# Kernel optimization log

Measured on AMD Instinct MI355X. Metric: run time of the kernel, lower is better.

## Reference

```python
import jax, jax.numpy as jnp
import numpy as np

B, T, H, L, V = 256, 201, 512, 3, 100
SOS_IDX = 1


def setup_inputs() -> dict:
    key = jax.random.key(0)
    ks = jax.random.split(key, 9)
    s = 1.0 / np.sqrt(H)  # torch LSTM init scale
    return {
        "feat": jax.random.normal(ks[0], (B, H), jnp.float32),
        "target_seq": jax.random.randint(ks[1], (B, T), 0, V, jnp.int64),
        "embed": jax.random.normal(ks[2], (V, H), jnp.float32) * 0.02,
        "W_ih": jax.random.uniform(ks[3], (L, 4 * H, H), jnp.float32, -s, s),
        "W_hh": jax.random.uniform(ks[4], (L, 4 * H, H), jnp.float32, -s, s),
        "b_ih": jax.random.uniform(ks[5], (L, 4 * H), jnp.float32, -s, s),
        "b_hh": jax.random.uniform(ks[6], (L, 4 * H), jnp.float32, -s, s),
        "proj_W": jax.random.normal(ks[7], (V, H), jnp.float32) * 0.02,
        "proj_b": jnp.zeros((V,), jnp.float32),
    }


def reference(feat, target_seq, embed, W_ih, W_hh, b_ih, b_hh, proj_W, proj_b):
    n_layers = W_ih.shape[0]
    bsz = feat.shape[0]
    hid = feat.shape[1]

    # hidden init = resnet feature repeated across layers; cell = zeros
    h0 = jnp.broadcast_to(feat[None], (n_layers, bsz, hid))
    c0 = jnp.zeros_like(h0)

    # teacher forcing: embed target tokens for t = 1..T-1 -> [T-1, B, H]
    x_seq = embed[target_seq[:, 1:].T]

    def step(carry, x_t):
        h, c = carry  # [L, B, H] each
        inp = x_t
        h_new, c_new = [], []
        for l in range(n_layers):  # static small loop over layers
            gates = inp @ W_ih[l].T + b_ih[l] + h[l] @ W_hh[l].T + b_hh[l]
            i, f, g, o = jnp.split(gates, 4, axis=-1)  # torch gate order ifgo
            cl = jax.nn.sigmoid(f) * c[l] + jax.nn.sigmoid(i) * jnp.tanh(g)
            hl = jax.nn.sigmoid(o) * jnp.tanh(cl)
            h_new.append(hl)
            c_new.append(cl)
            inp = hl
        return (jnp.stack(h_new), jnp.stack(c_new)), inp

    _, outs = jax.lax.scan(step, (h0, c0), x_seq)  # outs: [T-1, B, H]

    # first output slot is the raw SOS embedding (as in the torch code)
    start = jnp.broadcast_to(embed[SOS_IDX][None, None, :], (1, bsz, hid))
    res = jnp.concatenate([start, outs], axis=0)  # [T, B, H]
    res = jnp.transpose(res, (1, 0, 2))           # [B, T, H]
    logits = res @ proj_W.T + proj_b              # [B, T, V]
    return jnp.transpose(logits, (0, 2, 1))       # [B, V, T]
```

## Files before the change

kernel.cpp:

```cpp
#include <hip/hip_runtime.h>
#include <hip/hip_bf16.h>
#include <stdint.h>

typedef __attribute__((ext_vector_type(8))) __bf16 bf16x8;
typedef __attribute__((ext_vector_type(8))) short short8;
typedef __attribute__((ext_vector_type(4))) float f32x4;
typedef __attribute__((ext_vector_type(16))) float f32x16;

#define NB 256
#define NT 201
#define NTS 200
#define NH 512
#define NV 100
#define NG 2048
#define NK2 1024

static __device__ __forceinline__ unsigned short f2bf(float f) {
  union { float f; uint32_t u; } v; v.f = f;
  uint32_t u = v.u;
  return (unsigned short)((u + 0x7fffu + ((u >> 16) & 1u)) >> 16);
}

__global__ void prep_kernel(const float* __restrict__ Wih, const float* __restrict__ Whh,
                            const float* __restrict__ bih, const float* __restrict__ bhh,
                            const float* __restrict__ projW, const float* __restrict__ embed,
                            const float* __restrict__ feat,
                            unsigned short* __restrict__ Wr, float* __restrict__ br,
                            unsigned short* __restrict__ WpB, unsigned short* __restrict__ sos,
                            unsigned short* __restrict__ hfeat)
{
  int idx = blockIdx.x * 256 + threadIdx.x;
  if (idx < 786432) {
    int l = idx >> 18;
    int rem = idx & 262143;
    int col = rem >> 7;
    int ch = rem & 127;
    int g = col & 3, j = col >> 2;
    int srow = g * 512 + j;
    int k0 = ch * 8;
    const float* src = (k0 < 512) ? (Wih + ((size_t)l * NG + srow) * NH + k0)
                                  : (Whh + ((size_t)l * NG + srow) * NH + (k0 - 512));
    union { short8 v; unsigned short u[8]; } o;
#pragma unroll
    for (int q = 0; q < 8; ++q) o.u[q] = f2bf(src[q]);
    *reinterpret_cast<short8*>(Wr + ((size_t)l * NG + col) * NK2 + k0) = o.v;
  } else if (idx < 792576) {
    int e = idx - 786432;
    int l = e >> 11;
    int col = e & 2047;
    int srow = (col & 3) * 512 + (col >> 2);
    br[e] = bih[l * NG + srow] + bhh[l * NG + srow];
  } else if (idx < 799744) {
    int e = idx - 792576;
    int row = e >> 6, sl = e & 63;
    int k0 = sl * 8;
    union { short8 v; unsigned short u[8]; } o;
    if (row < NV) {
      const float* src = projW + (size_t)row * NH + k0;
#pragma unroll
      for (int q = 0; q < 8; ++q) o.u[q] = f2bf(src[q]);
    } else {
#pragma unroll
      for (int q = 0; q < 8; ++q) o.u[q] = 0;
    }
    *reinterpret_cast<short8*>(WpB + (size_t)row * NH + k0) = o.v;
  } else if (idx < 799808) {
    int e = idx - 799744;
    int k0 = e * 8;
    union { short8 v; unsigned short u[8]; } o;
#pragma unroll
    for (int q = 0; q < 8; ++q) o.u[q] = f2bf(embed[NH + k0 + q]);
    *reinterpret_cast<short8*>(sos + k0) = o.v;
  } else if (idx < 816192) {
    int e = idx - 799808;
    int k0 = e * 8;
    union { short8 v; unsigned short u[8]; } o;
#pragma unroll
    for (int q = 0; q < 8; ++q) o.u[q] = f2bf(feat[k0 + q]);
    *reinterpret_cast<short8*>(hfeat + k0) = o.v;
  }
}

__global__ void embed_kernel(const int* __restrict__ tgt, const float* __restrict__ embed,
                             unsigned short* __restrict__ xemb)
{
  int idx = blockIdx.x * 256 + threadIdx.x;
  int r = idx >> 6, ch = idx & 63;
  int t = r >> 8, b = r & 255;
  int tok = tgt[b * NT + t + 1];
  const float* src = embed + (size_t)tok * NH + ch * 8;
  union { short8 v; unsigned short u[8]; } o;
#pragma unroll
  for (int q = 0; q < 8; ++q) o.u[q] = f2bf(src[q]);
  *reinterpret_cast<short8*>(xemb + (size_t)r * NH + ch * 8) = o.v;
}

template<int I, bool DEV>
struct Iss {
  static __device__ __forceinline__ void go(bf16x8* f, const unsigned short* p) {
    if constexpr (DEV)
      asm volatile("global_load_dwordx4 %0, %1, off offset:%c2 sc1"
                   : "=v"(f[I]) : "v"(p), "i"(I * 32));
    else
      asm volatile("global_load_dwordx4 %0, %1, off offset:%c2"
                   : "=v"(f[I]) : "v"(p), "i"(I * 32));
    Iss<I + 1, DEV>::go(f, p);
  }
};
template<bool DEV>
struct Iss<32, DEV> { static __device__ __forceinline__ void go(bf16x8*, const unsigned short*) {} };

static __device__ __forceinline__ unsigned ld_poll(const unsigned* p) {
  unsigned r;
  asm volatile("global_load_dword %0, %1, off sc1\n\ts_waitcnt vmcnt(0)"
               : "=v"(r) : "v"(p) : "memory");
  return r;
}

static __device__ __forceinline__ void sig_add(unsigned* p) {
  unsigned one = 1u;
  asm volatile("global_atomic_add %0, %1, off sc1" :: "v"(p), "v"(one) : "memory");
}

static __device__ __forceinline__ void stsc1(unsigned short* p, unsigned short v) {
  asm volatile("global_store_short %0, %1, off sc1" :: "v"(p), "v"(v) : "memory");
}

#define MFMA __builtin_amdgcn_mfma_f32_32x32x16_bf16
#define GW(N) do { asm volatile("s_waitcnt vmcnt(" #N ")"); \
                   __builtin_amdgcn_sched_barrier(0); } while (0)
#define VMCNT0 asm volatile("s_waitcnt vmcnt(0)" ::: "memory")

__global__ __launch_bounds__(128, 1)
void lstm_scan(const unsigned short* __restrict__ Wr, const float* __restrict__ br,
               const unsigned short* __restrict__ xemb, unsigned short* __restrict__ out0,
               unsigned short* __restrict__ out1, const unsigned short* __restrict__ hfeat,
               unsigned* __restrict__ bar)
{
  extern __shared__ char lds[];
  const int bid = blockIdx.x;
  const int c = bid & 7, wgi = bid >> 3;
  const int tid = threadIdx.x;
  const int wv = tid >> 6, l = tid & 63;
  const int lm = l & 31, lh = l >> 5;
  const int lh16 = lh * 16, lh8 = lh * 8;
  const int sampG = c * 32 + lm;
  const int colL = wv * 32 + lm;
  const int colG = wgi * 64 + colL;
  const bool isg = ((colG & 3) == 2);
  const int j = colG >> 2;
  const int xorr = (colL & 7) << 4;
  const char* wbase = lds + colL * 2048;
  unsigned* barc = bar + c * 64;

  const unsigned short* xs_[3] = { xemb, out0, out1 };
  unsigned short* os_[3] = { out0, out1, out0 };

  bf16x8 f[32];
  f32x16 a0a, a0b, a1a, a1b;

#define XM(ks) \
  a0a = MFMA(f[ks],     *(const bf16x8*)(wbase + (((ks)*32 + lh16) ^ xorr)),     a0a, 0,0,0); \
  a0b = MFMA(f[(ks)+1], *(const bf16x8*)(wbase + ((((ks)+1)*32 + lh16) ^ xorr)), a0b, 0,0,0);
#define HM(ks) \
  a1a = MFMA(f[ks],     *(const bf16x8*)(wbase + ((1024 + (ks)*32 + lh16) ^ xorr)),     a1a, 0,0,0); \
  a1b = MFMA(f[(ks)+1], *(const bf16x8*)(wbase + ((1024 + ((ks)+1)*32 + lh16) ^ xorr)), a1b, 0,0,0);

  for (int layer = 0; layer < 3; ++layer) {
    __syncthreads();
    if (layer == 2) __threadfence();
    const unsigned short* wsrc = Wr + ((size_t)layer * NG + (size_t)wgi * 64) * NK2;
    for (int e = tid; e < 8192; e += 128) {
      int row = e >> 7, sl = e & 127;
      int byte = row * 2048 + ((sl * 16) ^ ((row & 7) << 4));
      *reinterpret_cast<short8*>(lds + byte) =
          *reinterpret_cast<const short8*>(wsrc + (size_t)row * NK2 + sl * 8);
    }
    __syncthreads();

    const float bias = br[layer * NG + colG];
    float cst[16];
#pragma unroll
    for (int r = 0; r < 16; ++r) cst[r] = 0.f;

    const unsigned short* xsrc = xs_[layer];
    unsigned short* osrc = os_[layer];

    Iss<0, false>::go(f, xsrc + (size_t)sampG * NH + lh8);
#pragma unroll
    for (int i = 0; i < 16; ++i) { a0a[i] = 0.f; a0b[i] = 0.f; }
    GW(24); XM(0) XM(2) XM(4) XM(6)
    GW(16); XM(8) XM(10) XM(12) XM(14)
    GW(8);  XM(16) XM(18) XM(20) XM(22)
    GW(0);  XM(24) XM(26) XM(28) XM(30)

    for (int t = 0; t < NTS; ++t) {
      if (t) {
        unsigned tgt = 32u * (unsigned)(layer * NTS + t);
        while (ld_poll(barc) < tgt) {}
      }
      const unsigned short* hr = (t == 0)
          ? (hfeat + (size_t)sampG * NH + lh8)
          : (osrc + ((size_t)(t - 1) * NB + sampG) * NH + lh8);
      Iss<0, true>::go(f, hr);
#pragma unroll
      for (int i = 0; i < 16; ++i) { a1a[i] = 0.f; a1b[i] = 0.f; }
      GW(24); HM(0) HM(2) HM(4) HM(6)
      GW(16); HM(8) HM(10) HM(12) HM(14)
      GW(8);  HM(16) HM(18) HM(20) HM(22)
      GW(0);  HM(24) HM(26) HM(28) HM(30)

      unsigned short* orow = osrc + (size_t)t * NB * NH;
#pragma unroll
      for (int r = 0; r < 16; ++r) {
        float x = a0a[r] + a0b[r] + a1a[r] + a1b[r] + bias;
        float xx = isg ? (x + x) : x;
        float sgm = 1.f / (1.f + __expf(-xx));
        float a = isg ? (sgm + sgm - 1.f) : sgm;
        float f1 = __shfl_xor(a, 1);
        float u2 = __shfl_xor(a, 2);
        float o3 = __shfl_xor(a, 3);
        float cn = __builtin_fmaf(f1, cst[r], a * u2);
        cst[r] = cn;
        float e2 = __expf(-2.f * cn);
        float th = 2.f / (1.f + e2) - 1.f;
        float hv = o3 * th;
        if ((l & 3) == 0) {
          int m = (r & 3) + 8 * (r >> 2) + 4 * lh;
          stsc1(orow + (size_t)(c * 32 + m) * NH + j, f2bf(hv));
        }
      }

      VMCNT0;
      __syncthreads();
      if (tid == 0) sig_add(barc);

      if (t < NTS - 1) {
        Iss<0, false>::go(f, xsrc + ((size_t)(t + 1) * NB + sampG) * NH + lh8);
#pragma unroll
        for (int i = 0; i < 16; ++i) { a0a[i] = 0.f; a0b[i] = 0.f; }
        GW(24); XM(0) XM(2) XM(4) XM(6)
        GW(16); XM(8) XM(10) XM(12) XM(14)
        GW(8);  XM(16) XM(18) XM(20) XM(22)
        GW(0);  XM(24) XM(26) XM(28) XM(30)
      }
    }
  }
}

__global__ __launch_bounds__(256)
void proj_kernel(const unsigned short* __restrict__ WpB, const unsigned short* __restrict__ outL,
                 const unsigned short* __restrict__ sos, const float* __restrict__ pb,
                 float* __restrict__ dout)
{
  extern __shared__ char plds[];
  const int b = blockIdx.x, tid = threadIdx.x;
  const int wv = tid >> 6, l = tid & 63;
  const int ln = l & 15, lk = l >> 4;
  for (int e = tid; e < 7168; e += 256) {
    int row = e >> 6, sl = e & 63;
    int byte = row * 1024 + ((sl * 16) ^ ((row & 7) << 4));
    *reinterpret_cast<short8*>(plds + byte) =
        *reinterpret_cast<const short8*>(WpB + (size_t)row * NH + sl * 8);
  }
  __syncthreads();
  for (int nt = wv; nt < 13; nt += 4) {
    int tt = nt * 16 + ln;
    const unsigned short* rowp = (tt == 0 || tt > 200) ? sos
        : outL + ((size_t)(tt - 1) * NB + b) * NH;
    bf16x8 Bfr[16];
#pragma unroll
    for (int ks = 0; ks < 16; ++ks)
      Bfr[ks] = *reinterpret_cast<const bf16x8*>(rowp + ks * 32 + lk * 8);
    for (int mt = 0; mt < 7; ++mt) {
      f32x4 acc;
#pragma unroll
      for (int i = 0; i < 4; ++i) acc[i] = 0.f;
#pragma unroll
      for (int ks = 0; ks < 16; ++ks) {
        int row = mt * 16 + ln;
        int byte = row * 1024 + (((ks * 64) + lk * 16) ^ ((row & 7) << 4));
        bf16x8 a = *reinterpret_cast<const bf16x8*>(plds + byte);
        acc = __builtin_amdgcn_mfma_f32_16x16x32_bf16(a, Bfr[ks], acc, 0, 0, 0);
      }
#pragma unroll
      for (int r = 0; r < 4; ++r) {
        int v = mt * 16 + lk * 4 + r;
        if (v < NV && tt < NT)
          dout[((size_t)b * NV + v) * NT + tt] = acc[r] + pb[v];
      }
    }
  }
}

extern "C" void kernel_launch(void* const* d_in, const int* in_sizes, int n_in,
                              void* d_out, int out_size, void* d_ws, size_t ws_size,
                              hipStream_t stream)
{
  const float* feat  = (const float*)d_in[0];
  const int*   tgt   = (const int*)  d_in[1];
  const float* embed = (const float*)d_in[2];
  const float* Wih   = (const float*)d_in[3];
  const float* Whh   = (const float*)d_in[4];
  const float* bih   = (const float*)d_in[5];
  const float* bhh   = (const float*)d_in[6];
  const float* projW = (const float*)d_in[7];
  const float* pb    = (const float*)d_in[8];
  float* out = (float*)d_out;

  char* ws = (char*)d_ws;
  size_t off = 0;
  auto alloc = [&](size_t bytes) {
    char* p = ws + off;
    off = (off + bytes + 255) & ~(size_t)255;
    return p;
  };
  unsigned short* Wr    = (unsigned short*)alloc((size_t)3 * NG * NK2 * 2);
  float*          br    = (float*)         alloc((size_t)3 * NG * 4);
  unsigned short* WpB   = (unsigned short*)alloc((size_t)112 * NH * 2);
  unsigned short* sos   = (unsigned short*)alloc((size_t)NH * 2);
  unsigned short* hfeat = (unsigned short*)alloc((size_t)NB * NH * 2);
  unsigned short* xemb  = (unsigned short*)alloc((size_t)NTS * NB * NH * 2);
  unsigned short* out0  = (unsigned short*)alloc((size_t)NTS * NB * NH * 2);
  unsigned*       bar   = (unsigned*)      alloc(2048);
  unsigned short* out1 = xemb;

  hipMemsetAsync(bar, 0, 2048, stream);

  hipFuncSetAttribute((const void*)lstm_scan, hipFuncAttributeMaxDynamicSharedMemorySize, 131072);
  hipFuncSetAttribute((const void*)proj_kernel, hipFuncAttributeMaxDynamicSharedMemorySize, 114688);

  prep_kernel<<<3189, 256, 0, stream>>>(Wih, Whh, bih, bhh, projW, embed, feat,
                                        Wr, br, WpB, sos, hfeat);
  embed_kernel<<<12800, 256, 0, stream>>>(tgt, embed, xemb);
  lstm_scan<<<256, 128, 131072, stream>>>(Wr, br, xemb, out0, out1, hfeat, bar);
  proj_kernel<<<256, 256, 114688, stream>>>(WpB, out0, sos, pb, out);
}
```

Baseline: 4.736 ms.

## Replace atomic counter barrier with per-block flags and staged vectorized h stores

Each workgroup now writes a monotonically increasing flag to its own slot instead of atomically incrementing a shared counter. Waiters poll all 32 flags in parallel across lanes and use a wave vote. The scattered 2-byte hidden-state stores are staged through a small LDS tile and written as 8-byte coalesced stores. The LDS weight swizzle is widened to 32 rows to reduce bank conflicts. This adds an extra __syncthreads and 2KB of LDS per step, in exchange for cutting atomic contention and the per-step store count on the critical recurrence path.

```diff
diff --git a/kernel.cpp b/kernel.cpp
--- a/kernel.cpp
+++ b/kernel.cpp
@@ -6,6 +6,7 @@
 typedef __attribute__((ext_vector_type(8))) short short8;
 typedef __attribute__((ext_vector_type(4))) float f32x4;
 typedef __attribute__((ext_vector_type(16))) float f32x16;
+typedef __attribute__((ext_vector_type(2))) unsigned int uint2v;
 
 #define NB 256
 #define NT 201
@@ -110,20 +111,17 @@
 template<bool DEV>
 struct Iss<32, DEV> { static __device__ __forceinline__ void go(bf16x8*, const unsigned short*) {} };
 
-static __device__ __forceinline__ unsigned ld_poll(const unsigned* p) {
+static __device__ __forceinline__ unsigned ld_flag(const unsigned* p) {
   unsigned r;
   asm volatile("global_load_dword %0, %1, off sc1\n\ts_waitcnt vmcnt(0)"
                : "=v"(r) : "v"(p) : "memory");
   return r;
 }
-
-static __device__ __forceinline__ void sig_add(unsigned* p) {
-  unsigned one = 1u;
-  asm volatile("global_atomic_add %0, %1, off sc1" :: "v"(p), "v"(one) : "memory");
-}
-
-static __device__ __forceinline__ void stsc1(unsigned short* p, unsigned short v) {
-  asm volatile("global_store_short %0, %1, off sc1" :: "v"(p), "v"(v) : "memory");
+static __device__ __forceinline__ void st_flag(unsigned* p, unsigned v) {
+  asm volatile("global_store_dword %0, %1, off sc1" :: "v"(p), "v"(v) : "memory");
+}
+static __device__ __forceinline__ void st8_sc1(unsigned short* p, uint2v v) {
+  asm volatile("global_store_dwordx2 %0, %1, off sc1" :: "v"(p), "v"(v) : "memory");
 }
 
 #define MFMA __builtin_amdgcn_mfma_f32_32x32x16_bf16
@@ -138,6 +136,7 @@
                unsigned* __restrict__ bar)
 {
   extern __shared__ char lds[];
+  unsigned short* tile = (unsigned short*)(lds + 131072);
   const int bid = blockIdx.x;
   const int c = bid & 7, wgi = bid >> 3;
   const int tid = threadIdx.x;
@@ -148,10 +147,11 @@
   const int colL = wv * 32 + lm;
   const int colG = wgi * 64 + colL;
   const bool isg = ((colG & 3) == 2);
-  const int j = colG >> 2;
-  const int xorr = (colL & 7) << 4;
+  const int jl = colL >> 2;
+  const int xorr = (colL & 31) << 4;
   const char* wbase = lds + colL * 2048;
-  unsigned* barc = bar + c * 64;
+  unsigned* flags = bar + c * 32;
+  const unsigned* myf = flags + lm;
 
   const unsigned short* xs_[3] = { xemb, out0, out1 };
   unsigned short* os_[3] = { out0, out1, out0 };
@@ -172,7 +172,7 @@
     const unsigned short* wsrc = Wr + ((size_t)layer * NG + (size_t)wgi * 64) * NK2;
     for (int e = tid; e < 8192; e += 128) {
       int row = e >> 7, sl = e & 127;
-      int byte = row * 2048 + ((sl * 16) ^ ((row & 7) << 4));
+      int byte = row * 2048 + ((sl * 16) ^ ((row & 31) << 4));
       *reinterpret_cast<short8*>(lds + byte) =
           *reinterpret_cast<const short8*>(wsrc + (size_t)row * NK2 + sl * 8);
     }
@@ -196,8 +196,11 @@
 
     for (int t = 0; t < NTS; ++t) {
       if (t) {
-        unsigned tgt = 32u * (unsigned)(layer * NTS + t);
-        while (ld_poll(barc) < tgt) {}
+        unsigned tgt = (unsigned)(layer * NTS + t);
+        while (true) {
+          unsigned v = ld_flag(myf);
+          if (__all((int)(v >= tgt))) break;
+        }
       }
       const unsigned short* hr = (t == 0)
           ? (hfeat + (size_t)sampG * NH + lh8)
@@ -210,7 +213,6 @@
       GW(8);  HM(16) HM(18) HM(20) HM(22)
       GW(0);  HM(24) HM(26) HM(28) HM(30)
 
-      unsigned short* orow = osrc + (size_t)t * NB * NH;
 #pragma unroll
       for (int r = 0; r < 16; ++r) {
         float x = a0a[r] + a0b[r] + a1a[r] + a1b[r] + bias;
@@ -227,13 +229,20 @@
         float hv = o3 * th;
         if ((l & 3) == 0) {
           int m = (r & 3) + 8 * (r >> 2) + 4 * lh;
-          stsc1(orow + (size_t)(c * 32 + m) * NH + j, f2bf(hv));
+          tile[m * 16 + jl] = f2bf(hv);
         }
       }
-
+      __syncthreads();
+      {
+        int m = tid >> 2, ch = tid & 3;
+        uint2v v = *reinterpret_cast<const uint2v*>(tile + tid * 4);
+        unsigned short* gp = osrc + (size_t)t * NB * NH
+                           + (size_t)(c * 32 + m) * NH + wgi * 16 + ch * 4;
+        st8_sc1(gp, v);
+      }
       VMCNT0;
       __syncthreads();
-      if (tid == 0) sig_add(barc);
+      if (tid == 0) st_flag(bar + c * 32 + wgi, (unsigned)(layer * NTS + t + 1));
 
       if (t < NTS - 1) {
         Iss<0, false>::go(f, xsrc + ((size_t)(t + 1) * NB + sampG) * NH + lh8);
@@ -327,12 +336,12 @@
 
   hipMemsetAsync(bar, 0, 2048, stream);
 
-  hipFuncSetAttribute((const void*)lstm_scan, hipFuncAttributeMaxDynamicSharedMemorySize, 131072);
+  hipFuncSetAttribute((const void*)lstm_scan, hipFuncAttributeMaxDynamicSharedMemorySize, 133120);
   hipFuncSetAttribute((const void*)proj_kernel, hipFuncAttributeMaxDynamicSharedMemorySize, 114688);
 
   prep_kernel<<<3189, 256, 0, stream>>>(Wih, Whh, bih, bhh, projW, embed, feat,
                                         Wr, br, WpB, sos, hfeat);
   embed_kernel<<<12800, 256, 0, stream>>>(tgt, embed, xemb);
-  lstm_scan<<<256, 128, 131072, stream>>>(Wr, br, xemb, out0, out1, hfeat, bar);
+  lstm_scan<<<256, 128, 133120, stream>>>(Wr, br, xemb, out0, out1, hfeat, bar);
   proj_kernel<<<256, 256, 114688, stream>>>(WpB, out0, sos, pb, out);
 }
```

After: 4.800 ms. Within noise of the previous version (+1.3%).
